# Optimization experiments

Measured on AMD Instinct MI355X. Metric: run time of the kernel, lower is better.

## Reference

```python
import jax, jax.numpy as jnp
import numpy as np

B, C, H, W = 16, 192, 64, 64
L = 256           # number of quantization levels (len(sos.unique_values))
EXTREMA = 10.0    # codebook support roughly [-extrema, extrema]


def setup_inputs() -> dict:
    key = jax.random.key(0)
    k1, k2, k3 = jax.random.split(key, 3)
    inputs = jax.random.normal(k1, (B, C, H, W), dtype=jnp.float32) * 3.0
    means = jax.random.normal(k2, (B, C, H, W), dtype=jnp.float32)
    # sorted codebook of unique quantizer output values (sos.unique_values)
    raw = jax.random.uniform(k3, (L,), dtype=jnp.float32,
                             minval=-EXTREMA, maxval=EXTREMA)
    unique_values = jnp.sort(raw)
    return {"inputs": inputs, "means": means, "unique_values": unique_values}


def _nearest_symbols(v, unique_values):
    # Parallel binary search over the sorted codebook; equivalent to the
    # original per-element argmin(|keys - x|) in transform_map.
    L_ = unique_values.shape[0]
    idx = jnp.searchsorted(unique_values, v)          # in [0, L]
    idx = jnp.clip(idx, 1, L_ - 1)
    left = unique_values[idx - 1]
    right = unique_values[idx]
    # on ties, argmin picks the lower index -> use <=
    return jnp.where(jnp.abs(v - left) <= jnp.abs(v - right), idx - 1, idx)


def reference(inputs, means, unique_values):
    # quantize(mode='symbols'): subtract means, snap to nearest codebook
    # value, map value -> integer symbol via the sorted codebook.
    v = inputs - means
    symbols = _nearest_symbols(v, unique_values)      # int32 [B,C,H,W]
    # dequantize: symbol -> float codebook value (map_cdf_sos), add means.
    dequant = unique_values[symbols] + means          # float32 [B,C,H,W]
    return dequant, symbols
```

## Files before the change

kernel.cpp:

```cpp
#include <hip/hip_runtime.h>
#include <math.h>


#define LVL 256
#define NB  2048

__device__ __forceinline__ int lb_bj(const int* s_bj, int x) {
    int lo = 0, hi = LVL;
    #pragma unroll
    for (int s = 0; s < 8; ++s) {
        int mid = (lo + hi) >> 1;
        bool r = (s_bj[mid] < x);
        lo = r ? mid + 1 : lo;
        hi = r ? hi : mid;
    }
    return lo;
}

__global__ __launch_bounds__(256) void agc_build(
    const float* __restrict__ uv, float* __restrict__ ws)
{
    __shared__ float s_uv[LVL];
    __shared__ float s_mid[LVL];
    __shared__ int   s_bj[LVL];
    int tid = threadIdx.x;
    s_uv[tid] = uv[tid];
    __syncthreads();
    float mid = (tid < LVL - 1) ? 0.5f * (s_uv[tid] + s_uv[tid + 1]) : INFINITY;
    s_mid[tid] = mid;
    __syncthreads();
    float lo = s_mid[0], hi = s_mid[LVL - 2];
    float scale = (float)NB / (hi - lo);
    float f = (mid - lo) * scale;
    f = fminf(fmaxf(f, 0.0f), (float)(NB - 1));
    s_bj[tid] = (tid < LVL - 1) ? (int)f : 0x7fffffff;
    __syncthreads();

    if (blockIdx.x == 0) {
        float4 p;
        p.x = s_mid[tid];
        p.y = s_uv[tid];
        p.z = (tid < LVL - 1) ? s_uv[tid + 1] : s_uv[LVL - 1];
        p.w = 0.0f;
        ((float4*)ws)[tid] = p;
        if (tid == 0) { ws[9216] = lo; ws[9217] = scale; }
    }

    float4* T = (float4*)(ws + 1024);
    int stride = gridDim.x * blockDim.x;
    for (int m = blockIdx.x * blockDim.x + tid; m < NB; m += stride) {
        int l0 = lb_bj(s_bj, m);
        int l1 = lb_bj(s_bj, m + 1);
        int cnt = l1 - l0;
        int b = l0 > 255 ? 255 : l0;
        float4 e;
        e.x = s_mid[b];
        e.y = s_uv[b];
        e.z = (b < LVL - 1) ? s_uv[b + 1] : s_uv[LVL - 1];
        e.w = __int_as_float(b | (cnt << 16));
        T[m] = e;
    }
}

__device__ __forceinline__ int lb_mid(const float4* s_pack, float v) {
    int lo = 0, hi = LVL;
    #pragma unroll
    for (int s = 0; s < 8; ++s) {
        int mid = (lo + hi) >> 1;
        bool r = (s_pack[mid].x < v);
        lo = r ? mid + 1 : lo;
        hi = r ? hi : mid;
    }
    return lo;
}

__global__ __launch_bounds__(256) void agc_quant(
    const float* __restrict__ inputs, const float* __restrict__ means,
    const float* __restrict__ ws,
    float* __restrict__ out_deq, float* __restrict__ out_sym,
    int n4, int n)
{
    __shared__ float4 s_T[NB];
    __shared__ float4 s_pack[LVL];
    int tid = threadIdx.x;
    const float4* gT = (const float4*)(ws + 1024);
    #pragma unroll
    for (int m = tid; m < NB; m += 256) s_T[m] = gT[m];
    s_pack[tid] = ((const float4*)ws)[tid];
    float lo = ws[9216], scale = ws[9217];
    __syncthreads();

    const float4* in4 = (const float4*)inputs;
    const float4* mn4 = (const float4*)means;
    float4* dq4 = (float4*)out_deq;
    float4* sy4 = (float4*)out_sym;
    const float fNBm1 = (float)(NB - 1);

    int nth = gridDim.x * blockDim.x;
    int gid = blockIdx.x * blockDim.x + tid;

    for (int base_i = gid; base_i < n4; base_i += 2 * nth) {
        int i0 = base_i;
        int i1 = base_i + nth;
        bool h1 = (i1 < n4);

        float4 a0 = in4[i0], b0 = mn4[i0];
        float4 a1 = make_float4(0, 0, 0, 0), b1 = make_float4(0, 0, 0, 0);
        if (h1) { a1 = in4[i1]; b1 = mn4[i1]; }

        float v[8], me[8];
        v[0] = a0.x - b0.x; v[1] = a0.y - b0.y; v[2] = a0.z - b0.z; v[3] = a0.w - b0.w;
        v[4] = a1.x - b1.x; v[5] = a1.y - b1.y; v[6] = a1.z - b1.z; v[7] = a1.w - b1.w;
        me[0] = b0.x; me[1] = b0.y; me[2] = b0.z; me[3] = b0.w;
        me[4] = b1.x; me[5] = b1.y; me[6] = b1.z; me[7] = b1.w;

        float4 t[8];
        #pragma unroll
        for (int k = 0; k < 8; ++k) {
            float f = (v[k] - lo) * scale;
            f = fminf(fmaxf(f, 0.0f), fNBm1);
            t[k] = s_T[(int)f];
        }

        float dq[8], sy[8];
        #pragma unroll
        for (int k = 0; k < 8; ++k) {
            int meta = __float_as_int(t[k].w);
            int b   = meta & 0xffff;
            int cnt = meta >> 16;
            bool take1 = (cnt > 0) && (t[k].x < v[k]);
            int   sym = b + (take1 ? 1 : 0);
            float val = take1 ? t[k].z : t[k].y;
            if (take1 && cnt >= 2) {
                float4 p = s_pack[b + 1];
                bool take2 = (p.x < v[k]);
                sym += take2 ? 1 : 0;
                val  = take2 ? p.z : val;
                int kk = 2;
                while (take2 && kk < cnt) {
                    float4 p2 = s_pack[b + kk];
                    take2 = (p2.x < v[k]);
                    sym += take2 ? 1 : 0;
                    val  = take2 ? p2.z : val;
                    ++kk;
                }
            }
            sy[k] = (float)sym;
            dq[k] = val + me[k];
        }

        dq4[i0] = make_float4(dq[0], dq[1], dq[2], dq[3]);
        sy4[i0] = make_float4(sy[0], sy[1], sy[2], sy[3]);
        if (h1) {
            dq4[i1] = make_float4(dq[4], dq[5], dq[6], dq[7]);
            sy4[i1] = make_float4(sy[4], sy[5], sy[6], sy[7]);
        }
    }

    if (blockIdx.x == 0 && tid == 0) {
        for (int j = n4 * 4; j < n; ++j) {
            float m = means[j];
            float vv = inputs[j] - m;
            int s = lb_mid(s_pack, vv);
            out_sym[j] = (float)s;
            out_deq[j] = s_pack[s].y + m;
        }
    }
}

extern "C" void kernel_launch(void* const* d_in, const int* in_sizes, int n_in,
                              void* d_out, int out_size, void* d_ws, size_t ws_size,
                              hipStream_t stream) {
    const float* inputs = (const float*)d_in[0];
    const float* means  = (const float*)d_in[1];
    const float* uv     = (const float*)d_in[2];

    int n  = in_sizes[0];
    int n4 = n / 4;

    float* out     = (float*)d_out;
    float* out_deq = out;
    float* out_sym = out + n;
    float* ws      = (float*)d_ws;

    agc_build<<<16, 256, 0, stream>>>(uv, ws);

    agc_quant<<<1024, 256, 0, stream>>>(
        inputs, means, ws, out_deq, out_sym, n4, n);
}
```

Before: 187.9 us.

## Halve bucket table, prefetch next tile, use nontemporal stores, double grid

The LDS bucket table shrinks from 2048 to 1024 entries, which halves shared memory per block and allows more resident blocks. The main loop now handles one float4 per iteration and loads the next iteration's inputs before computing the current one, a software-pipelining prefetch. Outputs are written with nontemporal stores to avoid cache pollution, and the grid is doubled. Coarser buckets may raise the per-bucket level count, lengthening the linear fix-up scan for some elements.

```diff
diff --git a/kernel.cpp b/kernel.cpp
--- a/kernel.cpp
+++ b/kernel.cpp
@@ -3,7 +3,9 @@
 
 
 #define LVL 256
-#define NB  2048
+#define NB  1024
+
+typedef float vfloat4 __attribute__((ext_vector_type(4)));
 
 __device__ __forceinline__ int lb_bj(const int* s_bj, int x) {
     int lo = 0, hi = LVL;
@@ -43,7 +45,7 @@
         p.z = (tid < LVL - 1) ? s_uv[tid + 1] : s_uv[LVL - 1];
         p.w = 0.0f;
         ((float4*)ws)[tid] = p;
-        if (tid == 0) { ws[9216] = lo; ws[9217] = scale; }
+        if (tid == 0) { ws[5120] = lo; ws[5121] = scale; }
     }
 
     float4* T = (float4*)(ws + 1024);
@@ -74,6 +76,50 @@
     return lo;
 }
 
+__device__ __forceinline__ void agc_resolve4(
+    const float4& a, const float4& b,
+    const float4* s_T, const float4* s_pack,
+    float lo, float scale, float fNBm1,
+    vfloat4& dq_o, vfloat4& sy_o)
+{
+    float v[4]  = {a.x - b.x, a.y - b.y, a.z - b.z, a.w - b.w};
+    float me[4] = {b.x, b.y, b.z, b.w};
+
+    float4 t[4];
+    #pragma unroll
+    for (int k = 0; k < 4; ++k) {
+        float f = (v[k] - lo) * scale;
+        f = fminf(fmaxf(f, 0.0f), fNBm1);
+        t[k] = s_T[(int)f];
+    }
+
+    float dq[4], sy[4];
+    #pragma unroll
+    for (int k = 0; k < 4; ++k) {
+        int meta = __float_as_int(t[k].w);
+        int bb  = meta & 0xffff;
+        int cnt = meta >> 16;
+        bool take1 = (cnt > 0) && (t[k].x < v[k]);
+        int   sym = bb + (take1 ? 1 : 0);
+        float val = take1 ? t[k].z : t[k].y;
+        if (take1 && cnt >= 2) {
+            int kk = 1;
+            bool take2 = true;
+            while (take2 && kk < cnt) {
+                float4 p = s_pack[bb + kk];
+                take2 = (p.x < v[k]);
+                sym += take2 ? 1 : 0;
+                val  = take2 ? p.z : val;
+                ++kk;
+            }
+        }
+        sy[k] = (float)sym;
+        dq[k] = val + me[k];
+    }
+    dq_o = (vfloat4){dq[0], dq[1], dq[2], dq[3]};
+    sy_o = (vfloat4){sy[0], sy[1], sy[2], sy[3]};
+}
+
 __global__ __launch_bounds__(256) void agc_quant(
     const float* __restrict__ inputs, const float* __restrict__ means,
     const float* __restrict__ ws,
@@ -87,73 +133,33 @@
     #pragma unroll
     for (int m = tid; m < NB; m += 256) s_T[m] = gT[m];
     s_pack[tid] = ((const float4*)ws)[tid];
-    float lo = ws[9216], scale = ws[9217];
+    float lo = ws[5120], scale = ws[5121];
     __syncthreads();
 
     const float4* in4 = (const float4*)inputs;
     const float4* mn4 = (const float4*)means;
-    float4* dq4 = (float4*)out_deq;
-    float4* sy4 = (float4*)out_sym;
+    vfloat4* dq4 = (vfloat4*)out_deq;
+    vfloat4* sy4 = (vfloat4*)out_sym;
     const float fNBm1 = (float)(NB - 1);
 
     int nth = gridDim.x * blockDim.x;
-    int gid = blockIdx.x * blockDim.x + tid;
+    int i = blockIdx.x * blockDim.x + tid;
 
-    for (int base_i = gid; base_i < n4; base_i += 2 * nth) {
-        int i0 = base_i;
-        int i1 = base_i + nth;
-        bool h1 = (i1 < n4);
+    if (i < n4) {
+        float4 a = in4[i], b = mn4[i];
+        while (true) {
+            int inext = i + nth;
+            bool vnext = (inext < n4);
+            float4 an, bn;
+            if (vnext) { an = in4[inext]; bn = mn4[inext]; }
 
-        float4 a0 = in4[i0], b0 = mn4[i0];
-        float4 a1 = make_float4(0, 0, 0, 0), b1 = make_float4(0, 0, 0, 0);
-        if (h1) { a1 = in4[i1]; b1 = mn4[i1]; }
+            vfloat4 dq, sy;
+            agc_resolve4(a, b, s_T, s_pack, lo, scale, fNBm1, dq, sy);
+            __builtin_nontemporal_store(dq, &dq4[i]);
+            __builtin_nontemporal_store(sy, &sy4[i]);
 
-        float v[8], me[8];
-        v[0] = a0.x - b0.x; v[1] = a0.y - b0.y; v[2] = a0.z - b0.z; v[3] = a0.w - b0.w;
-        v[4] = a1.x - b1.x; v[5] = a1.y - b1.y; v[6] = a1.z - b1.z; v[7] = a1.w - b1.w;
-        me[0] = b0.x; me[1] = b0.y; me[2] = b0.z; me[3] = b0.w;
-        me[4] = b1.x; me[5] = b1.y; me[6] = b1.z; me[7] = b1.w;
-
-        float4 t[8];
-        #pragma unroll
-        for (int k = 0; k < 8; ++k) {
-            float f = (v[k] - lo) * scale;
-            f = fminf(fmaxf(f, 0.0f), fNBm1);
-            t[k] = s_T[(int)f];
-        }
-
-        float dq[8], sy[8];
-        #pragma unroll
-        for (int k = 0; k < 8; ++k) {
-            int meta = __float_as_int(t[k].w);
-            int b   = meta & 0xffff;
-            int cnt = meta >> 16;
-            bool take1 = (cnt > 0) && (t[k].x < v[k]);
-            int   sym = b + (take1 ? 1 : 0);
-            float val = take1 ? t[k].z : t[k].y;
-            if (take1 && cnt >= 2) {
-                float4 p = s_pack[b + 1];
-                bool take2 = (p.x < v[k]);
-                sym += take2 ? 1 : 0;
-                val  = take2 ? p.z : val;
-                int kk = 2;
-                while (take2 && kk < cnt) {
-                    float4 p2 = s_pack[b + kk];
-                    take2 = (p2.x < v[k]);
-                    sym += take2 ? 1 : 0;
-                    val  = take2 ? p2.z : val;
-                    ++kk;
-                }
-            }
-            sy[k] = (float)sym;
-            dq[k] = val + me[k];
-        }
-
-        dq4[i0] = make_float4(dq[0], dq[1], dq[2], dq[3]);
-        sy4[i0] = make_float4(sy[0], sy[1], sy[2], sy[3]);
-        if (h1) {
-            dq4[i1] = make_float4(dq[4], dq[5], dq[6], dq[7]);
-            sy4[i1] = make_float4(sy[4], sy[5], sy[6], sy[7]);
+            if (!vnext) break;
+            i = inext; a = an; b = bn;
         }
     }
 
@@ -183,8 +189,8 @@
     float* out_sym = out + n;
     float* ws      = (float*)d_ws;
 
-    agc_build<<<16, 256, 0, stream>>>(uv, ws);
+    agc_build<<<8, 256, 0, stream>>>(uv, ws);
 
-    agc_quant<<<1024, 256, 0, stream>>>(
+    agc_quant<<<2048, 256, 0, stream>>>(
         inputs, means, ws, out_deq, out_sym, n4, n);
 }
```

Result: no change. 185.5 us (-1.3%).
